# Kernel tuning notes

Measured on AMD Instinct MI355X. Metric: run time of the kernel, lower is better.

## Reference

```python
import jax, jax.numpy as jnp
import numpy as np

N_NODES = 100000
N_EDGES = 1600000
IN_DIM, HID_DIM, OUT_DIM = 128, 128, 64


def setup_inputs() -> dict:
    key = jax.random.key(0)
    k1, k2, k3, k4 = jax.random.split(key, 4)
    x = jax.random.normal(k1, (N_NODES, IN_DIM), dtype=jnp.float32)
    edge_index = jax.random.randint(k2, (2, N_EDGES), 0, N_NODES, dtype=jnp.int64)
    W1 = jax.random.normal(k3, (IN_DIM, HID_DIM), dtype=jnp.float32) * (1.0 / np.sqrt(IN_DIM))
    b1 = jnp.zeros((HID_DIM,), dtype=jnp.float32)
    W2 = jax.random.normal(k4, (HID_DIM, OUT_DIM), dtype=jnp.float32) * (1.0 / np.sqrt(HID_DIM))
    b2 = jnp.zeros((OUT_DIM,), dtype=jnp.float32)
    return {"x": x, "edge_index": edge_index, "W1": W1, "b1": b1, "W2": W2, "b2": b2}


def _gcn_conv(x, W, b, src, dst, num_nodes):
    # PyG GCNConv (normalize=True): h = D^{-1/2} A_hat D^{-1/2} (x W) + b
    h = x @ W  # [N, out]
    ones = jnp.ones(src.shape[0], dtype=h.dtype)
    deg = jax.ops.segment_sum(ones, dst, num_segments=num_nodes)  # in-degree incl self-loops
    dinv = jnp.where(deg > 0, jax.lax.rsqrt(deg), jnp.zeros_like(deg))
    norm = dinv[src] * dinv[dst]  # [E]
    msg = h[src] * norm[:, None]  # gather + scale, [E, out]
    out = jax.ops.segment_sum(msg, dst, num_segments=num_nodes)  # scatter-add
    return out + b


def reference(x, edge_index, W1, b1, W2, b2):
    n = x.shape[0]
    loop = jnp.arange(n, dtype=edge_index.dtype)
    src = jnp.concatenate([edge_index[0], loop])  # add_self_loops=True
    dst = jnp.concatenate([edge_index[1], loop])
    h = jax.nn.elu(_gcn_conv(x, W1, b1, src, dst, n))
    out = jax.nn.elu(_gcn_conv(h, W2, b2, src, dst, n))
    return out
```

## Files before the change

kernel.cpp:

```cpp
#include <hip/hip_runtime.h>
#include <hip/hip_bf16.h>

#define N_NODES 100000
#define N_EDGES 1600000
#define IN_DIM  128
#define HID_DIM 128
#define OUT_DIM 64
#define SCAN_CHUNK 1024
#define NBLK_SCAN ((N_NODES + SCAN_CHUNK - 1) / SCAN_CHUNK)

typedef __attribute__((ext_vector_type(8))) short short8;
typedef __attribute__((ext_vector_type(4))) float floatx4;

__device__ __forceinline__ float eluf(float x) { return x > 0.0f ? x : expm1f(x); }
__device__ __forceinline__ unsigned short bfbits(float f) {
    union { __hip_bfloat16 h; unsigned short u; } c; c.h = __float2bfloat16(f); return c.u;
}
__device__ __forceinline__ unsigned packbf(float a, float b) {
    return (unsigned)bfbits(a) | ((unsigned)bfbits(b) << 16);
}
__device__ __forceinline__ float lo16(unsigned u) { return __uint_as_float(u << 16); }
__device__ __forceinline__ float hi16(unsigned u) { return __uint_as_float(u & 0xffff0000u); }

__global__ void k_detect(const int* __restrict__ ei, int* __restrict__ flag) {
    __shared__ int acc;
    if (threadIdx.x == 0) acc = 0;
    __syncthreads();
    int v = 0;
    for (int e = threadIdx.x; e < 1024; e += 256) v |= ei[2 * e + 1];
    atomicOr(&acc, v);
    __syncthreads();
    if (threadIdx.x == 0) flag[0] = (acc == 0) ? 1 : 0;
}
__device__ __forceinline__ int esrc(const int* ei, int e, int is64) {
    return is64 ? ei[2 * e] : ei[e];
}
__device__ __forceinline__ int edst(const int* ei, int e, int is64) {
    return is64 ? ei[2 * (N_EDGES + e)] : ei[N_EDGES + e];
}

__global__ void k_deg_pos(const int* __restrict__ ei, const int* __restrict__ flag,
                          int* __restrict__ deg, unsigned short* __restrict__ epos) {
    int e = blockIdx.x * blockDim.x + threadIdx.x;
    if (e >= N_EDGES) return;
    int d = edst(ei, e, flag[0]);
    epos[e] = (unsigned short)atomicAdd(&deg[d], 1);
}
__global__ void k_scan1(const int* __restrict__ deg, int* __restrict__ rowStart,
                        int* __restrict__ bsum, float* __restrict__ dinv) {
    __shared__ int sd[256];
    int t = threadIdx.x, blk = blockIdx.x;
    int i0 = blk * SCAN_CHUNK + t * 4;
    int d0 = (i0 + 0 < N_NODES) ? deg[i0 + 0] : 0;
    int d1 = (i0 + 1 < N_NODES) ? deg[i0 + 1] : 0;
    int d2 = (i0 + 2 < N_NODES) ? deg[i0 + 2] : 0;
    int d3 = (i0 + 3 < N_NODES) ? deg[i0 + 3] : 0;
    if (i0 + 0 < N_NODES) dinv[i0 + 0] = rsqrtf((float)(d0 + 1));
    if (i0 + 1 < N_NODES) dinv[i0 + 1] = rsqrtf((float)(d1 + 1));
    if (i0 + 2 < N_NODES) dinv[i0 + 2] = rsqrtf((float)(d2 + 1));
    if (i0 + 3 < N_NODES) dinv[i0 + 3] = rsqrtf((float)(d3 + 1));
    int s4 = d0 + d1 + d2 + d3;
    sd[t] = s4;
    __syncthreads();
    int acc = s4;
    for (int off = 1; off < 256; off <<= 1) {
        int v = (t >= off) ? sd[t - off] : 0;
        __syncthreads();
        acc += v; sd[t] = acc;
        __syncthreads();
    }
    int excl = acc - s4;
    if (i0 + 0 < N_NODES) rowStart[i0 + 0] = excl;
    if (i0 + 1 < N_NODES) rowStart[i0 + 1] = excl + d0;
    if (i0 + 2 < N_NODES) rowStart[i0 + 2] = excl + d0 + d1;
    if (i0 + 3 < N_NODES) rowStart[i0 + 3] = excl + d0 + d1 + d2;
    if (t == 255) bsum[blk] = acc;
}
__global__ void k_scan2(int* __restrict__ bsum, int* __restrict__ rowStartN) {
    __shared__ int sd[128];
    int t = threadIdx.x;
    int v = (t < NBLK_SCAN) ? bsum[t] : 0;
    sd[t] = v;
    __syncthreads();
    int acc = v;
    for (int off = 1; off < 128; off <<= 1) {
        int u = (t >= off) ? sd[t - off] : 0;
        __syncthreads();
        acc += u; sd[t] = acc;
        __syncthreads();
    }
    if (t < NBLK_SCAN) bsum[t] = acc - v;
    if (t == NBLK_SCAN - 1) rowStartN[0] = acc;
}
__global__ void k_scan3(int* __restrict__ rowStart, const int* __restrict__ bsum) {
    int i = blockIdx.x * blockDim.x + threadIdx.x;
    if (i < N_NODES) rowStart[i] += bsum[i >> 10];
}
__global__ void k_fill(const int* __restrict__ ei, const int* __restrict__ flag,
                       const int* __restrict__ rowStart, const unsigned short* __restrict__ epos,
                       int* __restrict__ csr) {
    int e = blockIdx.x * blockDim.x + threadIdx.x;
    if (e >= N_EDGES) return;
    int is64 = flag[0];
    int s = esrc(ei, e, is64), d = edst(ei, e, is64);
    csr[rowStart[d] + (int)epos[e]] = s;
}

__global__ void k_cast_x(const float4* __restrict__ x4, uint2* __restrict__ xb) {
    int i = blockIdx.x * blockDim.x + threadIdx.x;
    if (i >= N_NODES * (IN_DIM / 4)) return;
    float4 v = x4[i];
    uint2 o = { packbf(v.x, v.y), packbf(v.z, v.w) };
    xb[i] = o;
}

__launch_bounds__(256)
__global__ void k_gather1(const unsigned* __restrict__ xb, const float* __restrict__ dinv,
                          const int* __restrict__ row, const int* __restrict__ csr,
                          unsigned* __restrict__ agg) {
    int w = (blockIdx.x * blockDim.x + threadIdx.x) >> 6;
    int lane = threadIdx.x & 63;
    if (w >= N_NODES) return;
    int beg = row[w], end = row[w + 1];
    float dd = dinv[w];
    unsigned sv = xb[w * 64 + lane];
    float ax = lo16(sv) * dd, ay = hi16(sv) * dd;
    int j = beg;
    for (; j + 8 <= end; j += 8) {
        int s[8]; float wd[8]; unsigned u[8];
#pragma unroll
        for (int q = 0; q < 8; q++) s[q] = csr[j + q];
#pragma unroll
        for (int q = 0; q < 8; q++) wd[q] = dinv[s[q]];
#pragma unroll
        for (int q = 0; q < 8; q++) u[q] = xb[s[q] * 64 + lane];
#pragma unroll
        for (int q = 0; q < 8; q++) { ax += lo16(u[q]) * wd[q]; ay += hi16(u[q]) * wd[q]; }
    }
    for (; j + 2 <= end; j += 2) {
        int s0 = csr[j], s1 = csr[j + 1];
        float w0 = dinv[s0], w1 = dinv[s1];
        unsigned u0 = xb[s0 * 64 + lane];
        unsigned u1 = xb[s1 * 64 + lane];
        ax += lo16(u0) * w0 + lo16(u1) * w1;
        ay += hi16(u0) * w0 + hi16(u1) * w1;
    }
    if (j < end) {
        int s0 = csr[j]; float w0 = dinv[s0];
        unsigned u0 = xb[s0 * 64 + lane];
        ax += lo16(u0) * w0; ay += hi16(u0) * w0;
    }
    agg[w * 64 + lane] = packbf(ax * dd, ay * dd);
}

__launch_bounds__(256)
__global__ void k_gather2(const unsigned* __restrict__ h2, const float* __restrict__ dinv,
                          const int* __restrict__ row, const int* __restrict__ csr,
                          const float* __restrict__ b2, float* __restrict__ out) {
    int w = (blockIdx.x * blockDim.x + threadIdx.x) >> 5;
    int p = threadIdx.x & 31;
    if (w >= N_NODES) return;
    float2 bias = *(const float2*)(b2 + 2 * p);
    int beg = row[w], end = row[w + 1];
    float dd = dinv[w];
    unsigned sv = h2[w * 32 + p];
    float ax = lo16(sv) * dd, ay = hi16(sv) * dd;
    int j = beg;
    for (; j + 8 <= end; j += 8) {
        int s[8]; float wd[8]; unsigned u[8];
#pragma unroll
        for (int q = 0; q < 8; q++) s[q] = csr[j + q];
#pragma unroll
        for (int q = 0; q < 8; q++) wd[q] = dinv[s[q]];
#pragma unroll
        for (int q = 0; q < 8; q++) u[q] = h2[s[q] * 32 + p];
#pragma unroll
        for (int q = 0; q < 8; q++) { ax += lo16(u[q]) * wd[q]; ay += hi16(u[q]) * wd[q]; }
    }
    for (; j + 2 <= end; j += 2) {
        int s0 = csr[j], s1 = csr[j + 1];
        float w0 = dinv[s0], w1 = dinv[s1];
        unsigned u0 = h2[s0 * 32 + p];
        unsigned u1 = h2[s1 * 32 + p];
        ax += lo16(u0) * w0 + lo16(u1) * w1;
        ay += hi16(u0) * w0 + hi16(u1) * w1;
    }
    if (j < end) {
        int s0 = csr[j]; float w0 = dinv[s0];
        unsigned u0 = h2[s0 * 32 + p];
        ax += lo16(u0) * w0; ay += hi16(u0) * w0;
    }
    ax *= dd; ay *= dd;
    float2 r = { eluf(ax + bias.x), eluf(ay + bias.y) };
    *(float2*)(out + w * OUT_DIM + 2 * p) = r;
}

__launch_bounds__(256)
__global__ void k_gemm1_mfma(unsigned* __restrict__ agg, const float* __restrict__ W1,
                             const float* __restrict__ b1, int nblk) {
    __shared__ short w1p[4][8][64][8];
    int t = threadIdx.x;
    for (int idx = t; idx < 8192; idx += 256) {
        int j2 = idx & 3, l = (idx >> 2) & 63, ct = (idx >> 8) & 7, kk = idx >> 11;
        int k = kk * 32 + (l >> 4) * 8 + j2 * 2;
        int c = ct * 16 + (l & 15);
        ((unsigned*)w1p)[idx] = packbf(W1[k * HID_DIM + c], W1[(k + 1) * HID_DIM + c]);
    }
    int lane = t & 63, wave = t >> 6;
    int q = lane >> 4, m = lane & 15;
    floatx4 bias[8];
#pragma unroll
    for (int ct = 0; ct < 8; ct++) bias[ct] = *(const floatx4*)(b1 + ct * 16 + q * 4);
    __syncthreads();
    for (int blk = blockIdx.x * 4 + wave; blk < nblk; blk += gridDim.x * 4) {
        int r = blk * 16 + m;
        const short8* arow = (const short8*)(agg + r * 64);
        short8 bfr[4];
#pragma unroll
        for (int kk = 0; kk < 4; kk++) bfr[kk] = arow[kk * 4 + q];
        floatx4 acc[8];
#pragma unroll
        for (int ct = 0; ct < 8; ct++) acc[ct] = (floatx4)0.0f;
#pragma unroll
        for (int kk = 0; kk < 4; kk++)
#pragma unroll
            for (int ct = 0; ct < 8; ct++) {
                short8 af = *(const short8*)(&w1p[kk][ct][lane][0]);
                acc[ct] = __builtin_amdgcn_mfma_f32_16x16x32_bf16(af, bfr[kk], acc[ct], 0, 0, 0);
            }
        unsigned* hrow = agg + r * 64;
#pragma unroll
        for (int ct = 0; ct < 8; ct++) {
            uint2 o;
            o.x = packbf(eluf(acc[ct][0] + bias[ct][0]), eluf(acc[ct][1] + bias[ct][1]));
            o.y = packbf(eluf(acc[ct][2] + bias[ct][2]), eluf(acc[ct][3] + bias[ct][3]));
            *(uint2*)(hrow + ct * 8 + q * 2) = o;
        }
    }
}

__launch_bounds__(256)
__global__ void k_gemm2_mfma(const unsigned* __restrict__ h1, const float* __restrict__ W2,
                             unsigned* __restrict__ h2, int nblk) {
    __shared__ short w2p[4][4][64][8];
    int t = threadIdx.x;
    for (int idx = t; idx < 4096; idx += 256) {
        int j2 = idx & 3, l = (idx >> 2) & 63, ct = (idx >> 8) & 3, kk = idx >> 10;
        int k = kk * 32 + (l >> 4) * 8 + j2 * 2;
        int c = ct * 16 + (l & 15);
        ((unsigned*)w2p)[idx] = packbf(W2[k * OUT_DIM + c], W2[(k + 1) * OUT_DIM + c]);
    }
    int lane = t & 63, wave = t >> 6;
    int q = lane >> 4, m = lane & 15;
    __syncthreads();
    for (int blk = blockIdx.x * 4 + wave; blk < nblk; blk += gridDim.x * 4) {
        int r = blk * 16 + m;
        const short8* arow = (const short8*)(h1 + r * 64);
        short8 bfr[4];
#pragma unroll
        for (int kk = 0; kk < 4; kk++) bfr[kk] = arow[kk * 4 + q];
        floatx4 acc[4];
#pragma unroll
        for (int ct = 0; ct < 4; ct++) acc[ct] = (floatx4)0.0f;
#pragma unroll
        for (int kk = 0; kk < 4; kk++)
#pragma unroll
            for (int ct = 0; ct < 4; ct++) {
                short8 af = *(const short8*)(&w2p[kk][ct][lane][0]);
                acc[ct] = __builtin_amdgcn_mfma_f32_16x16x32_bf16(af, bfr[kk], acc[ct], 0, 0, 0);
            }
        unsigned* orow = h2 + r * 32;
#pragma unroll
        for (int ct = 0; ct < 4; ct++) {
            uint2 o;
            o.x = packbf(acc[ct][0], acc[ct][1]);
            o.y = packbf(acc[ct][2], acc[ct][3]);
            *(uint2*)(orow + ct * 8 + q * 2) = o;
        }
    }
}

extern "C" void kernel_launch(void* const* d_in, const int* in_sizes, int n_in,
                              void* d_out, int out_size, void* d_ws, size_t ws_size,
                              hipStream_t stream) {
    const float* x  = (const float*)d_in[0];
    const int*   ei = (const int*)d_in[1];
    const float* W1 = (const float*)d_in[2];
    const float* b1 = (const float*)d_in[3];
    const float* W2 = (const float*)d_in[4];
    const float* b2 = (const float*)d_in[5];

    const size_t OFF_FLAG = 0, OFF_DEG = 16, OFF_ROW = 100016, OFF_BSUM = 200032,
                 OFF_CSR = 200192, OFF_DINV = 1800192,
                 OFF_XB = 1900288,
                 OFF_AGG = 8300288;
    const size_t needed = (OFF_AGG + 6400000) * 4;
    if (ws_size < needed) return;

    int*      flag = (int*)d_ws + OFF_FLAG;
    int*      deg  = (int*)d_ws + OFF_DEG;
    int*      row  = (int*)d_ws + OFF_ROW;
    int*      bsum = (int*)d_ws + OFF_BSUM;
    int*      csr  = (int*)d_ws + OFF_CSR;
    float*    dinv = (float*)d_ws + OFF_DINV;
    unsigned* xb   = (unsigned*)d_ws + OFF_XB;
    unsigned* agg  = (unsigned*)d_ws + OFF_AGG;
    unsigned short* epos = (unsigned short*)agg;

    k_detect<<<1, 256, 0, stream>>>(ei, flag);
    hipMemsetAsync(deg, 0, N_NODES * sizeof(int), stream);
    k_deg_pos<<<(N_EDGES + 255) / 256, 256, 0, stream>>>(ei, flag, deg, epos);
    k_scan1<<<NBLK_SCAN, 256, 0, stream>>>(deg, row, bsum, dinv);
    k_scan2<<<1, 128, 0, stream>>>(bsum, row + N_NODES);
    k_scan3<<<(N_NODES + 255) / 256, 256, 0, stream>>>(row, bsum);
    k_fill<<<(N_EDGES + 255) / 256, 256, 0, stream>>>(ei, flag, row, epos, csr);

    k_cast_x<<<(N_NODES * (IN_DIM / 4) + 255) / 256, 256, 0, stream>>>(
        (const float4*)x, (uint2*)xb);

    k_gather1<<<(N_NODES * 64 + 255) / 256, 256, 0, stream>>>(xb, dinv, row, csr, agg);
    k_gemm1_mfma<<<1024, 256, 0, stream>>>(agg, W1, b1, N_NODES / 16);

    k_gemm2_mfma<<<1024, 256, 0, stream>>>(agg, W2, xb, N_NODES / 16);
    k_gather2<<<(N_NODES * 32 + 255) / 256, 256, 0, stream>>>(
        xb, dinv, row, csr, b2, (float*)d_out);
}
```

Measured before the change: 350.6 us.

## Switch storage to fp16, fuse degree count with x cast, batch edge kernels

Replaces bf16 storage and MFMA with fp16 (f16 MFMA, half conversions) across gathers and GEMMs. Merges the degree/position atomic kernel and the x cast kernel into one launch, with each thread handling four edges, and gives the CSR fill kernel four edges per thread too. Gather tails are simplified to a single-edge loop using fmaf. The aim is fewer launches and cheaper unpacking; fp16 range is narrower than bf16, so large values could overflow.

```diff
diff --git a/kernel.cpp b/kernel.cpp
--- a/kernel.cpp
+++ b/kernel.cpp
@@ -8,19 +8,21 @@
 #define OUT_DIM 64
 #define SCAN_CHUNK 1024
 #define NBLK_SCAN ((N_NODES + SCAN_CHUNK - 1) / SCAN_CHUNK)
-
-typedef __attribute__((ext_vector_type(8))) short short8;
+#define DEG_BLOCKS ((N_EDGES + 1023) / 1024)
+#define CAST_BLOCKS ((N_NODES * (IN_DIM / 4) + 255) / 256)
+
+typedef _Float16 half2v __attribute__((ext_vector_type(2)));
+typedef _Float16 half8  __attribute__((ext_vector_type(8)));
 typedef __attribute__((ext_vector_type(4))) float floatx4;
 
 __device__ __forceinline__ float eluf(float x) { return x > 0.0f ? x : expm1f(x); }
-__device__ __forceinline__ unsigned short bfbits(float f) {
-    union { __hip_bfloat16 h; unsigned short u; } c; c.h = __float2bfloat16(f); return c.u;
-}
-__device__ __forceinline__ unsigned packbf(float a, float b) {
-    return (unsigned)bfbits(a) | ((unsigned)bfbits(b) << 16);
-}
-__device__ __forceinline__ float lo16(unsigned u) { return __uint_as_float(u << 16); }
-__device__ __forceinline__ float hi16(unsigned u) { return __uint_as_float(u & 0xffff0000u); }
+__device__ __forceinline__ unsigned packh(float a, float b) {
+    union { _Float16 h[2]; unsigned u; } c;
+    c.h[0] = (_Float16)a; c.h[1] = (_Float16)b; return c.u;
+}
+__device__ __forceinline__ half2v as_h2(unsigned u) {
+    union { unsigned u; half2v h; } c; c.u = u; return c.h;
+}
 
 __global__ void k_detect(const int* __restrict__ ei, int* __restrict__ flag) {
     __shared__ int acc;
@@ -39,13 +41,37 @@
     return is64 ? ei[2 * (N_EDGES + e)] : ei[N_EDGES + e];
 }
 
-__global__ void k_deg_pos(const int* __restrict__ ei, const int* __restrict__ flag,
-                          int* __restrict__ deg, unsigned short* __restrict__ epos) {
-    int e = blockIdx.x * blockDim.x + threadIdx.x;
-    if (e >= N_EDGES) return;
-    int d = edst(ei, e, flag[0]);
-    epos[e] = (unsigned short)atomicAdd(&deg[d], 1);
-}
+__global__ void k_prolog(const int* __restrict__ ei, const int* __restrict__ flag,
+                         int* __restrict__ deg, unsigned short* __restrict__ epos,
+                         const float4* __restrict__ x4, uint2* __restrict__ xh) {
+    int b = blockIdx.x;
+    if (b < DEG_BLOCKS) {
+        int base = (b * 256 + threadIdx.x) * 4;
+        int is64 = flag[0];
+        unsigned short ep[4];
+#pragma unroll
+        for (int q = 0; q < 4; q++) {
+            int e = base + q;
+            if (e < N_EDGES) {
+                int d = edst(ei, e, is64);
+                ep[q] = (unsigned short)atomicAdd(&deg[d], 1);
+            } else ep[q] = 0;
+        }
+        if (base + 3 < N_EDGES) {
+            *(ushort4*)(epos + base) = make_ushort4(ep[0], ep[1], ep[2], ep[3]);
+        } else {
+#pragma unroll
+            for (int q = 0; q < 4; q++) if (base + q < N_EDGES) epos[base + q] = ep[q];
+        }
+    } else {
+        int i = (b - DEG_BLOCKS) * 256 + threadIdx.x;
+        if (i >= N_NODES * (IN_DIM / 4)) return;
+        float4 v = x4[i];
+        uint2 o = { packh(v.x, v.y), packh(v.z, v.w) };
+        xh[i] = o;
+    }
+}
+
 __global__ void k_scan1(const int* __restrict__ deg, int* __restrict__ rowStart,
                         int* __restrict__ bsum, float* __restrict__ dinv) {
     __shared__ int sd[256];
@@ -99,23 +125,20 @@
 __global__ void k_fill(const int* __restrict__ ei, const int* __restrict__ flag,
                        const int* __restrict__ rowStart, const unsigned short* __restrict__ epos,
                        int* __restrict__ csr) {
-    int e = blockIdx.x * blockDim.x + threadIdx.x;
-    if (e >= N_EDGES) return;
+    int base = (blockIdx.x * 256 + threadIdx.x) * 4;
     int is64 = flag[0];
-    int s = esrc(ei, e, is64), d = edst(ei, e, is64);
-    csr[rowStart[d] + (int)epos[e]] = s;
-}
-
-__global__ void k_cast_x(const float4* __restrict__ x4, uint2* __restrict__ xb) {
-    int i = blockIdx.x * blockDim.x + threadIdx.x;
-    if (i >= N_NODES * (IN_DIM / 4)) return;
-    float4 v = x4[i];
-    uint2 o = { packbf(v.x, v.y), packbf(v.z, v.w) };
-    xb[i] = o;
+#pragma unroll
+    for (int q = 0; q < 4; q++) {
+        int e = base + q;
+        if (e < N_EDGES) {
+            int s = esrc(ei, e, is64), d = edst(ei, e, is64);
+            csr[rowStart[d] + (int)epos[e]] = s;
+        }
+    }
 }
 
 __launch_bounds__(256)
-__global__ void k_gather1(const unsigned* __restrict__ xb, const float* __restrict__ dinv,
+__global__ void k_gather1(const unsigned* __restrict__ xh, const float* __restrict__ dinv,
                           const int* __restrict__ row, const int* __restrict__ csr,
                           unsigned* __restrict__ agg) {
     int w = (blockIdx.x * blockDim.x + threadIdx.x) >> 6;
@@ -123,8 +146,8 @@
     if (w >= N_NODES) return;
     int beg = row[w], end = row[w + 1];
     float dd = dinv[w];
-    unsigned sv = xb[w * 64 + lane];
-    float ax = lo16(sv) * dd, ay = hi16(sv) * dd;
+    half2v sv = as_h2(xh[w * 64 + lane]);
+    float ax = (float)sv[0] * dd, ay = (float)sv[1] * dd;
     int j = beg;
     for (; j + 8 <= end; j += 8) {
         int s[8]; float wd[8]; unsigned u[8];
@@ -133,24 +156,21 @@
 #pragma unroll
         for (int q = 0; q < 8; q++) wd[q] = dinv[s[q]];
 #pragma unroll
-        for (int q = 0; q < 8; q++) u[q] = xb[s[q] * 64 + lane];
-#pragma unroll
-        for (int q = 0; q < 8; q++) { ax += lo16(u[q]) * wd[q]; ay += hi16(u[q]) * wd[q]; }
-    }
-    for (; j + 2 <= end; j += 2) {
-        int s0 = csr[j], s1 = csr[j + 1];
-        float w0 = dinv[s0], w1 = dinv[s1];
-        unsigned u0 = xb[s0 * 64 + lane];
-        unsigned u1 = xb[s1 * 64 + lane];
-        ax += lo16(u0) * w0 + lo16(u1) * w1;
-        ay += hi16(u0) * w0 + hi16(u1) * w1;
-    }
-    if (j < end) {
+        for (int q = 0; q < 8; q++) u[q] = xh[s[q] * 64 + lane];
+#pragma unroll
+        for (int q = 0; q < 8; q++) {
+            half2v h = as_h2(u[q]);
+            ax = fmaf((float)h[0], wd[q], ax);
+            ay = fmaf((float)h[1], wd[q], ay);
+        }
+    }
+    for (; j < end; j++) {
         int s0 = csr[j]; float w0 = dinv[s0];
-        unsigned u0 = xb[s0 * 64 + lane];
-        ax += lo16(u0) * w0; ay += hi16(u0) * w0;
-    }
-    agg[w * 64 + lane] = packbf(ax * dd, ay * dd);
+        half2v h = as_h2(xh[s0 * 64 + lane]);
+        ax = fmaf((float)h[0], w0, ax);
+        ay = fmaf((float)h[1], w0, ay);
+    }
+    agg[w * 64 + lane] = packh(ax * dd, ay * dd);
 }
 
 __launch_bounds__(256)
@@ -163,8 +183,8 @@
     float2 bias = *(const float2*)(b2 + 2 * p);
     int beg = row[w], end = row[w + 1];
     float dd = dinv[w];
-    unsigned sv = h2[w * 32 + p];
-    float ax = lo16(sv) * dd, ay = hi16(sv) * dd;
+    half2v sv = as_h2(h2[w * 32 + p]);
+    float ax = (float)sv[0] * dd, ay = (float)sv[1] * dd;
     int j = beg;
     for (; j + 8 <= end; j += 8) {
         int s[8]; float wd[8]; unsigned u[8];
@@ -175,20 +195,17 @@
 #pragma unroll
         for (int q = 0; q < 8; q++) u[q] = h2[s[q] * 32 + p];
 #pragma unroll
-        for (int q = 0; q < 8; q++) { ax += lo16(u[q]) * wd[q]; ay += hi16(u[q]) * wd[q]; }
-    }
-    for (; j + 2 <= end; j += 2) {
-        int s0 = csr[j], s1 = csr[j + 1];
-        float w0 = dinv[s0], w1 = dinv[s1];
-        unsigned u0 = h2[s0 * 32 + p];
-        unsigned u1 = h2[s1 * 32 + p];
-        ax += lo16(u0) * w0 + lo16(u1) * w1;
-        ay += hi16(u0) * w0 + hi16(u1) * w1;
-    }
-    if (j < end) {
+        for (int q = 0; q < 8; q++) {
+            half2v h = as_h2(u[q]);
+            ax = fmaf((float)h[0], wd[q], ax);
+            ay = fmaf((float)h[1], wd[q], ay);
+        }
+    }
+    for (; j < end; j++) {
         int s0 = csr[j]; float w0 = dinv[s0];
-        unsigned u0 = h2[s0 * 32 + p];
-        ax += lo16(u0) * w0; ay += hi16(u0) * w0;
+        half2v h = as_h2(h2[s0 * 32 + p]);
+        ax = fmaf((float)h[0], w0, ax);
+        ay = fmaf((float)h[1], w0, ay);
     }
     ax *= dd; ay *= dd;
     float2 r = { eluf(ax + bias.x), eluf(ay + bias.y) };
@@ -198,13 +215,13 @@
 __launch_bounds__(256)
 __global__ void k_gemm1_mfma(unsigned* __restrict__ agg, const float* __restrict__ W1,
                              const float* __restrict__ b1, int nblk) {
-    __shared__ short w1p[4][8][64][8];
+    __shared__ _Float16 w1p[4][8][64][8];
     int t = threadIdx.x;
     for (int idx = t; idx < 8192; idx += 256) {
         int j2 = idx & 3, l = (idx >> 2) & 63, ct = (idx >> 8) & 7, kk = idx >> 11;
         int k = kk * 32 + (l >> 4) * 8 + j2 * 2;
         int c = ct * 16 + (l & 15);
-        ((unsigned*)w1p)[idx] = packbf(W1[k * HID_DIM + c], W1[(k + 1) * HID_DIM + c]);
+        ((unsigned*)w1p)[idx] = packh(W1[k * HID_DIM + c], W1[(k + 1) * HID_DIM + c]);
     }
     int lane = t & 63, wave = t >> 6;
     int q = lane >> 4, m = lane & 15;
@@ -214,8 +231,8 @@
     __syncthreads();
     for (int blk = blockIdx.x * 4 + wave; blk < nblk; blk += gridDim.x * 4) {
         int r = blk * 16 + m;
-        const short8* arow = (const short8*)(agg + r * 64);
-        short8 bfr[4];
+        const half8* arow = (const half8*)(agg + r * 64);
+        half8 bfr[4];
 #pragma unroll
         for (int kk = 0; kk < 4; kk++) bfr[kk] = arow[kk * 4 + q];
         floatx4 acc[8];
@@ -225,15 +242,15 @@
         for (int kk = 0; kk < 4; kk++)
 #pragma unroll
             for (int ct = 0; ct < 8; ct++) {
-                short8 af = *(const short8*)(&w1p[kk][ct][lane][0]);
-                acc[ct] = __builtin_amdgcn_mfma_f32_16x16x32_bf16(af, bfr[kk], acc[ct], 0, 0, 0);
+                half8 af = *(const half8*)(&w1p[kk][ct][lane][0]);
+                acc[ct] = __builtin_amdgcn_mfma_f32_16x16x32_f16(af, bfr[kk], acc[ct], 0, 0, 0);
             }
         unsigned* hrow = agg + r * 64;
 #pragma unroll
         for (int ct = 0; ct < 8; ct++) {
             uint2 o;
-            o.x = packbf(eluf(acc[ct][0] + bias[ct][0]), eluf(acc[ct][1] + bias[ct][1]));
-            o.y = packbf(eluf(acc[ct][2] + bias[ct][2]), eluf(acc[ct][3] + bias[ct][3]));
+            o.x = packh(eluf(acc[ct][0] + bias[ct][0]), eluf(acc[ct][1] + bias[ct][1]));
+            o.y = packh(eluf(acc[ct][2] + bias[ct][2]), eluf(acc[ct][3] + bias[ct][3]));
             *(uint2*)(hrow + ct * 8 + q * 2) = o;
         }
     }
@@ -242,21 +259,21 @@
 __launch_bounds__(256)
 __global__ void k_gemm2_mfma(const unsigned* __restrict__ h1, const float* __restrict__ W2,
                              unsigned* __restrict__ h2, int nblk) {
-    __shared__ short w2p[4][4][64][8];
+    __shared__ _Float16 w2p[4][4][64][8];
     int t = threadIdx.x;
     for (int idx = t; idx < 4096; idx += 256) {
         int j2 = idx & 3, l = (idx >> 2) & 63, ct = (idx >> 8) & 3, kk = idx >> 10;
         int k = kk * 32 + (l >> 4) * 8 + j2 * 2;
         int c = ct * 16 + (l & 15);
-        ((unsigned*)w2p)[idx] = packbf(W2[k * OUT_DIM + c], W2[(k + 1) * OUT_DIM + c]);
+        ((unsigned*)w2p)[idx] = packh(W2[k * OUT_DIM + c], W2[(k + 1) * OUT_DIM + c]);
     }
     int lane = t & 63, wave = t >> 6;
     int q = lane >> 4, m = lane & 15;
     __syncthreads();
     for (int blk = blockIdx.x * 4 + wave; blk < nblk; blk += gridDim.x * 4) {
         int r = blk * 16 + m;
-        const short8* arow = (const short8*)(h1 + r * 64);
-        short8 bfr[4];
+        const half8* arow = (const half8*)(h1 + r * 64);
+        half8 bfr[4];
 #pragma unroll
         for (int kk = 0; kk < 4; kk++) bfr[kk] = arow[kk * 4 + q];
         floatx4 acc[4];
@@ -266,15 +283,15 @@
         for (int kk = 0; kk < 4; kk++)
 #pragma unroll
             for (int ct = 0; ct < 4; ct++) {
-                short8 af = *(const short8*)(&w2p[kk][ct][lane][0]);
-                acc[ct] = __builtin_amdgcn_mfma_f32_16x16x32_bf16(af, bfr[kk], acc[ct], 0, 0, 0);
+                half8 af = *(const half8*)(&w2p[kk][ct][lane][0]);
+                acc[ct] = __builtin_amdgcn_mfma_f32_16x16x32_f16(af, bfr[kk], acc[ct], 0, 0, 0);
             }
         unsigned* orow = h2 + r * 32;
 #pragma unroll
         for (int ct = 0; ct < 4; ct++) {
             uint2 o;
-            o.x = packbf(acc[ct][0], acc[ct][1]);
-            o.y = packbf(acc[ct][2], acc[ct][3]);
+            o.x = packh(acc[ct][0], acc[ct][1]);
+            o.y = packh(acc[ct][2], acc[ct][3]);
             *(uint2*)(orow + ct * 8 + q * 2) = o;
         }
     }
@@ -303,25 +320,23 @@
     int*      bsum = (int*)d_ws + OFF_BSUM;
     int*      csr  = (int*)d_ws + OFF_CSR;
     float*    dinv = (float*)d_ws + OFF_DINV;
-    unsigned* xb   = (unsigned*)d_ws + OFF_XB;
+    unsigned* xh   = (unsigned*)d_ws + OFF_XB;
     unsigned* agg  = (unsigned*)d_ws + OFF_AGG;
     unsigned short* epos = (unsigned short*)agg;
 
     k_detect<<<1, 256, 0, stream>>>(ei, flag);
     hipMemsetAsync(deg, 0, N_NODES * sizeof(int), stream);
-    k_deg_pos<<<(N_EDGES + 255) / 256, 256, 0, stream>>>(ei, flag, deg, epos);
+    k_prolog<<<DEG_BLOCKS + CAST_BLOCKS, 256, 0, stream>>>(
+        ei, flag, deg, epos, (const float4*)x, (uint2*)xh);
     k_scan1<<<NBLK_SCAN, 256, 0, stream>>>(deg, row, bsum, dinv);
     k_scan2<<<1, 128, 0, stream>>>(bsum, row + N_NODES);
     k_scan3<<<(N_NODES + 255) / 256, 256, 0, stream>>>(row, bsum);
-    k_fill<<<(N_EDGES + 255) / 256, 256, 0, stream>>>(ei, flag, row, epos, csr);
-
-    k_cast_x<<<(N_NODES * (IN_DIM / 4) + 255) / 256, 256, 0, stream>>>(
-        (const float4*)x, (uint2*)xb);
-
-    k_gather1<<<(N_NODES * 64 + 255) / 256, 256, 0, stream>>>(xb, dinv, row, csr, agg);
+    k_fill<<<(N_EDGES / 4 + 255) / 256, 256, 0, stream>>>(ei, flag, row, epos, csr);
+
+    k_gather1<<<(N_NODES * 64 + 255) / 256, 256, 0, stream>>>(xh, dinv, row, csr, agg);
     k_gemm1_mfma<<<1024, 256, 0, stream>>>(agg, W1, b1, N_NODES / 16);
 
-    k_gemm2_mfma<<<1024, 256, 0, stream>>>(agg, W2, xb, N_NODES / 16);
+    k_gemm2_mfma<<<1024, 256, 0, stream>>>(agg, W2, xh, N_NODES / 16);
     k_gather2<<<(N_NODES * 32 + 255) / 256, 256, 0, stream>>>(
-        xb, dinv, row, csr, b2, (float*)d_out);
-}
+        xh, dinv, row, csr, b2, (float*)d_out);
+}
```

Measured after the change: 369.4 us. 5.4% more time.
